# Kernel optimization log

Hardware: AMD Instinct MI355X
Metric: run time of the kernel (lower is better)

## Reference

```python
import jax, jax.numpy as jnp
import numpy as np
import math

B, S, D, H, MLP, L = 4, 1024, 512, 8, 2048, 4
C = D // H  # head dim = 64
K_RATIO = 0.25
TOPK = max(1, min(S, int(math.ceil(K_RATIO * S))))  # 256
EPS = 1e-6


def layernorm(x, w, b):
    mu = jnp.mean(x, axis=-1, keepdims=True)
    var = jnp.mean(jnp.square(x - mu), axis=-1, keepdims=True)
    return (x - mu) * jax.lax.rsqrt(var + EPS) * w + b


def dwconv3(x, w):
    # x: (B, Ch, S), w: (Ch, 1, 3) depthwise conv, padding 1
    return jax.lax.conv_general_dilated(
        x, w, window_strides=(1,), padding=[(1, 1)],
        dimension_numbers=('NCH', 'OIH', 'NCH'),
        feature_group_count=x.shape[1])


def setup_inputs() -> dict:
    key = jax.random.key(0)
    ks = jax.random.split(key, 16)
    g = lambda k, shape, s=0.02: jax.random.normal(k, shape, jnp.float32) * s
    return {
        'x': jax.random.normal(ks[0], (B, S, D), jnp.float32),
        'pos_emb': g(ks[1], (1, S, D)),
        'ln1_w': jnp.ones((L, D), jnp.float32),
        'ln1_b': jnp.zeros((L, D), jnp.float32),
        'qkv_w': g(ks[2], (L, 3 * D, D)),
        'dw_w': g(ks[3], (L, 3 * D, 1, 3), 0.1),
        'temp': jnp.ones((L, H), jnp.float32),
        'proj_w': g(ks[4], (L, D, D)),
        'ln2_w': jnp.ones((L, D), jnp.float32),
        'ln2_b': jnp.zeros((L, D), jnp.float32),
        'mlp_w1': g(ks[5], (L, MLP, D)),
        'mlp_b1': g(ks[6], (L, MLP), 1e-6),
        'mlp_w2': g(ks[7], (L, D, MLP)),
        'mlp_b2': g(ks[8], (L, D), 1e-6),
        'lnf_w': jnp.ones((D,), jnp.float32),
        'lnf_b': jnp.zeros((D,), jnp.float32),
    }


def _block(x, ln1_w, ln1_b, qkv_w, dw_w, temp, proj_w, ln2_w, ln2_b,
           mlp_w1, mlp_b1, mlp_w2, mlp_b2):
    # x: (B, S, D)
    h = layernorm(x, ln1_w, ln1_b).swapaxes(1, 2)        # (B, D, S)
    qkv = jnp.einsum('od,bds->bos', qkv_w, h)            # (B, 3D, S) 1x1 conv
    qkv = dwconv3(qkv, dw_w)                             # depthwise k=3
    q, k, v = jnp.split(qkv, 3, axis=1)                  # each (B, D, S)
    # 'b (head c) s -> b head s c'
    to_heads = lambda t: t.reshape(B, H, C, S).transpose(0, 1, 3, 2)
    q, k, v = to_heads(q), to_heads(k), to_heads(v)      # (B, H, S, C)
    q = q / jnp.maximum(jnp.linalg.norm(q, axis=-1, keepdims=True), 1e-12)
    k = k / jnp.maximum(jnp.linalg.norm(k, axis=-1, keepdims=True), 1e-12)
    scores = jnp.einsum('bhsc,bhtc->bhst', q, k) * temp[None, :, None, None]
    # top-k per query row: keep entries >= k-th largest, mask rest to -inf
    kth = jax.lax.top_k(scores, TOPK)[0][..., -1:]       # (B, H, S, 1)
    sparse = jnp.where(scores >= kth, scores, -jnp.inf)
    sparse = jnp.clip(sparse, -10000.0, 10000.0)         # -inf -> -10000
    attn = jax.nn.softmax(sparse, axis=-1)
    out = jnp.einsum('bhst,bhtc->bhsc', attn, v)         # (B, H, S, C)
    out = out.transpose(0, 1, 3, 2).reshape(B, D, S)     # 'b head s c -> b (head c) s'
    out = jnp.einsum('od,bds->bos', proj_w, out)         # project_out 1x1 conv
    x = x + out.swapaxes(1, 2)                           # residual (dropout=0)
    y = layernorm(x, ln2_w, ln2_b)
    y = jax.nn.gelu(y @ mlp_w1.T + mlp_b1, approximate=False) @ mlp_w2.T + mlp_b2
    return x + y


def reference(x, pos_emb, ln1_w, ln1_b, qkv_w, dw_w, temp, proj_w,
              ln2_w, ln2_b, mlp_w1, mlp_b1, mlp_w2, mlp_b2, lnf_w, lnf_b):
    h = x + pos_emb
    for i in range(L):
        h = _block(h, ln1_w[i], ln1_b[i], qkv_w[i], dw_w[i], temp[i], proj_w[i],
                   ln2_w[i], ln2_b[i], mlp_w1[i], mlp_b1[i], mlp_w2[i], mlp_b2[i])
    return layernorm(h, lnf_w, lnf_b)
```

## Files before the change

kernel.cpp:

```cpp
#include <hip/hip_runtime.h>

#define NB   4
#define SEQ  1024
#define DIM  512
#define NH   8
#define HD   64
#define MLPD 2048
#define NL   4
#define TOPKK 256
#define QKVD 1536
#define QT   16
#define SCB  1032

typedef short bh8 __attribute__((ext_vector_type(8)));
typedef float f32x4 __attribute__((ext_vector_type(4)));

__device__ __forceinline__ float b2f(unsigned short v) {
    return __uint_as_float(((unsigned)v) << 16);
}
__device__ __forceinline__ unsigned short f2b(float f) {
    unsigned u = __float_as_uint(f);
    u += 0x7FFFu + ((u >> 16) & 1u);
    return (unsigned short)(u >> 16);
}
__device__ __forceinline__ float ldin(const void* p, size_t i, int bf) {
    return bf ? b2f(((const unsigned short*)p)[i]) : ((const float*)p)[i];
}
__device__ __forceinline__ float wave_sum(float v) {
#pragma unroll
    for (int m = 32; m; m >>= 1) v += __shfl_xor(v, m);
    return v;
}
__device__ __forceinline__ unsigned f2key16(unsigned short u) {
    return (u & 0x8000u) ? (unsigned)((~u) & 0xFFFFu) : (unsigned)(u | 0x8000u);
}
__device__ __forceinline__ unsigned short key16b(unsigned k) {
    return (k & 0x8000u) ? (unsigned short)(k & 0x7FFFu)
                         : (unsigned short)((~k) & 0xFFFFu);
}
__device__ __forceinline__ uint4 pack8(const float* __restrict__ p) {
    uint4 r;
    r.x = (unsigned)f2b(p[0]) | ((unsigned)f2b(p[1]) << 16);
    r.y = (unsigned)f2b(p[2]) | ((unsigned)f2b(p[3]) << 16);
    r.z = (unsigned)f2b(p[4]) | ((unsigned)f2b(p[5]) << 16);
    r.w = (unsigned)f2b(p[6]) | ((unsigned)f2b(p[7]) << 16);
    return r;
}
__device__ __forceinline__ void async16(unsigned short* lds, const unsigned short* g) {
    __builtin_amdgcn_global_load_lds(
        (const __attribute__((address_space(1))) unsigned int*)g,
        (__attribute__((address_space(3))) unsigned int*)lds, 16, 0, 0);
}


__global__ void detect_kernel(const unsigned short* __restrict__ ln1w,
                              int* __restrict__ flag) {
    if (threadIdx.x == 0 && blockIdx.x == 0)
        *flag = (ln1w[0] == 0x3F80u) ? 1 : 0;
}

__global__ __launch_bounds__(256) void wcvt_kernel(
    const void* __restrict__ W, unsigned short* __restrict__ out,
    int n, const int* __restrict__ dflag) {
    int bf = *dflag;
    int idx = blockIdx.x * 256 + threadIdx.x;
    if (idx < n) out[idx] = f2b(ldin(W, idx, bf));
}

__global__ __launch_bounds__(256) void addpos_kernel(
    const void* __restrict__ x, const void* __restrict__ pos,
    float* __restrict__ h, const int* __restrict__ dflag) {
    int bf = *dflag;
    int idx = blockIdx.x * 256 + threadIdx.x;
    int sd = idx & (SEQ * DIM - 1);
    h[idx] = ldin(x, idx, bf) + ldin(pos, sd, bf);
}

__global__ __launch_bounds__(256) void ln_kernel(
    const float* __restrict__ in, const void* __restrict__ w,
    const void* __restrict__ bb, size_t wo, unsigned short* __restrict__ out,
    const int* __restrict__ dflag) {
    int bf = *dflag;
    __shared__ float red[4];
    int row = blockIdx.x, tid = threadIdx.x;
    int lane = tid & 63, wid = tid >> 6;
    const float* p = in + (size_t)row * DIM;
    float x0 = p[tid], x1 = p[tid + 256];
    float s = wave_sum(x0 + x1);
    if (!lane) red[wid] = s;
    __syncthreads();
    float mean = (red[0] + red[1] + red[2] + red[3]) * (1.0f / DIM);
    float d0 = x0 - mean, d1 = x1 - mean;
    float q = wave_sum(d0 * d0 + d1 * d1);
    __syncthreads();
    if (!lane) red[wid] = q;
    __syncthreads();
    float var = (red[0] + red[1] + red[2] + red[3]) * (1.0f / DIM);
    float rs = rsqrtf(var + 1e-6f);
    unsigned short* o = out + (size_t)row * DIM;
    o[tid]       = f2b(d0 * rs * ldin(w, wo + tid, bf) + ldin(bb, wo + tid, bf));
    o[tid + 256] = f2b(d1 * rs * ldin(w, wo + tid + 256, bf) + ldin(bb, wo + tid + 256, bf));
}

__global__ __launch_bounds__(256) void lnf_kernel(
    const float* __restrict__ in, const void* __restrict__ w,
    const void* __restrict__ bb, void* __restrict__ out,
    const int* __restrict__ dflag) {
    int bf = *dflag;
    __shared__ float red[4];
    int row = blockIdx.x, tid = threadIdx.x;
    int lane = tid & 63, wid = tid >> 6;
    const float* p = in + (size_t)row * DIM;
    float x0 = p[tid], x1 = p[tid + 256];
    float s = wave_sum(x0 + x1);
    if (!lane) red[wid] = s;
    __syncthreads();
    float mean = (red[0] + red[1] + red[2] + red[3]) * (1.0f / DIM);
    float d0 = x0 - mean, d1 = x1 - mean;
    float q = wave_sum(d0 * d0 + d1 * d1);
    __syncthreads();
    if (!lane) red[wid] = q;
    __syncthreads();
    float var = (red[0] + red[1] + red[2] + red[3]) * (1.0f / DIM);
    float rs = rsqrtf(var + 1e-6f);
    float v0 = d0 * rs * ldin(w, tid, bf) + ldin(bb, tid, bf);
    float v1 = d1 * rs * ldin(w, tid + 256, bf) + ldin(bb, tid + 256, bf);
    size_t o = (size_t)row * DIM;
    if (bf) {
        ((unsigned short*)out)[o + tid]       = f2b(v0);
        ((unsigned short*)out)[o + tid + 256] = f2b(v1);
    } else {
        ((float*)out)[o + tid]       = v0;
        ((float*)out)[o + tid + 256] = v1;
    }
}

__global__ __launch_bounds__(256) void gemm_mfma_kernel(
    const unsigned short* __restrict__ A, const void* __restrict__ W, size_t wo,
    const void* __restrict__ bias, size_t bo, void* __restrict__ C,
    int M, int N, int K, int flags, const int* __restrict__ dflag) {
    int bf = *dflag;
    __shared__ unsigned short As[128 * 32];
    __shared__ unsigned short Bs[128 * 32];
    int tid = threadIdx.x;
    int w = tid >> 6, l = tid & 63;
    int n0 = blockIdx.x * 128, m0 = blockIdx.y * 128;
    int wm = (w >> 1) * 64, wn = (w & 1) * 64;
    int lq = l & 15, lk = l >> 4;

    int srow = w * 32 + (l >> 2);
    int cb = (l & 3) * 8;
    const unsigned short* aG = A + (size_t)(m0 + srow) * K + cb;
    size_t wb = wo + (size_t)(n0 + srow) * K + cb;
    unsigned short* sA0 = &As[w * 1024 + l * 8];
    unsigned short* sA1 = &As[w * 1024 + 512 + l * 8];
    unsigned short* sB0 = &Bs[w * 1024 + l * 8];
    unsigned short* sB1 = &Bs[w * 1024 + 512 + l * 8];

    f32x4 acc[4][4];
#pragma unroll
    for (int i = 0; i < 4; ++i)
#pragma unroll
        for (int j = 0; j < 4; ++j)
            acc[i][j] = (f32x4){0.f, 0.f, 0.f, 0.f};

    for (int k0 = 0; k0 < K; k0 += 32) {
        uint4 a0 = *(const uint4*)(aG + k0);
        uint4 a1 = *(const uint4*)(aG + 16 * K + k0);
        uint4 b0, b1;
        if (bf) {
            b0 = *(const uint4*)((const unsigned short*)W + wb + k0);
            b1 = *(const uint4*)((const unsigned short*)W + wb + 16 * K + k0);
        } else {
            b0 = pack8((const float*)W + wb + k0);
            b1 = pack8((const float*)W + wb + 16 * K + k0);
        }
        __syncthreads();
        *(uint4*)sA0 = a0;
        *(uint4*)sA1 = a1;
        *(uint4*)sB0 = b0;
        *(uint4*)sB1 = b1;
        __syncthreads();
        bh8 af[4], bw[4];
#pragma unroll
        for (int i = 0; i < 4; ++i) {
            af[i] = *(const bh8*)&As[(wm + i * 16 + lq) * 32 + lk * 8];
            bw[i] = *(const bh8*)&Bs[(wn + i * 16 + lq) * 32 + lk * 8];
        }
#pragma unroll
        for (int i = 0; i < 4; ++i)
#pragma unroll
            for (int j = 0; j < 4; ++j)
                acc[i][j] = __builtin_amdgcn_mfma_f32_16x16x32_bf16(
                    af[i], bw[j], acc[i][j], 0, 0, 0);
    }

    int lr4 = lk * 4;
#pragma unroll
    for (int i = 0; i < 4; ++i) {
#pragma unroll
        for (int j = 0; j < 4; ++j) {
            int n = n0 + wn + j * 16 + lq;
            float bv = (flags & 4) ? ldin(bias, bo + n, bf) : 0.0f;
#pragma unroll
            for (int r = 0; r < 4; ++r) {
                int m = m0 + wm + i * 16 + lr4 + r;
                float v = acc[i][j][r] + bv;
                if (flags & 2) v = 0.5f * v * (1.0f + erff(v * 0.70710678118654752f));
                size_t o = (size_t)m * N + n;
                if (flags & 1) ((float*)C)[o] += v;
                else           ((unsigned short*)C)[o] = f2b(v);
            }
        }
    }
}

__global__ __launch_bounds__(256) void gemm_mfma_n64_kernel(
    const unsigned short* __restrict__ A, const void* __restrict__ W, size_t wo,
    const void* __restrict__ bias, size_t bo, void* __restrict__ C,
    int M, int N, int K, int flags, const int* __restrict__ dflag) {
    int bf = *dflag;
    __shared__ unsigned short As[128 * 32];
    __shared__ unsigned short Bs[64 * 32];
    int tid = threadIdx.x;
    int w = tid >> 6, l = tid & 63;
    int n0 = blockIdx.x * 64, m0 = blockIdx.y * 128;
    int wm = (w >> 1) * 64, wn = (w & 1) * 32;
    int lq = l & 15, lk = l >> 4;

    int srowA = w * 32 + (l >> 2);
    int cb = (l & 3) * 8;
    const unsigned short* aG = A + (size_t)(m0 + srowA) * K + cb;
    int srowB = w * 16 + (l >> 2);
    size_t wb = wo + (size_t)(n0 + srowB) * K + cb;
    unsigned short* sA0 = &As[w * 1024 + l * 8];
    unsigned short* sA1 = &As[w * 1024 + 512 + l * 8];
    unsigned short* sB0 = &Bs[w * 512 + l * 8];

    f32x4 acc[4][2];
#pragma unroll
    for (int i = 0; i < 4; ++i) {
        acc[i][0] = (f32x4){0.f, 0.f, 0.f, 0.f};
        acc[i][1] = (f32x4){0.f, 0.f, 0.f, 0.f};
    }

    for (int k0 = 0; k0 < K; k0 += 32) {
        uint4 a0 = *(const uint4*)(aG + k0);
        uint4 a1 = *(const uint4*)(aG + 16 * K + k0);
        uint4 b0;
        if (bf) b0 = *(const uint4*)((const unsigned short*)W + wb + k0);
        else    b0 = pack8((const float*)W + wb + k0);
        __syncthreads();
        *(uint4*)sA0 = a0;
        *(uint4*)sA1 = a1;
        *(uint4*)sB0 = b0;
        __syncthreads();
        bh8 af[4], bw[2];
#pragma unroll
        for (int i = 0; i < 4; ++i)
            af[i] = *(const bh8*)&As[(wm + i * 16 + lq) * 32 + lk * 8];
        bw[0] = *(const bh8*)&Bs[(wn + lq) * 32 + lk * 8];
        bw[1] = *(const bh8*)&Bs[(wn + 16 + lq) * 32 + lk * 8];
#pragma unroll
        for (int i = 0; i < 4; ++i) {
            acc[i][0] = __builtin_amdgcn_mfma_f32_16x16x32_bf16(af[i], bw[0], acc[i][0], 0, 0, 0);
            acc[i][1] = __builtin_amdgcn_mfma_f32_16x16x32_bf16(af[i], bw[1], acc[i][1], 0, 0, 0);
        }
    }

    int lr4 = lk * 4;
#pragma unroll
    for (int i = 0; i < 4; ++i) {
#pragma unroll
        for (int j = 0; j < 2; ++j) {
            int n = n0 + wn + j * 16 + lq;
            float bv = (flags & 4) ? ldin(bias, bo + n, bf) : 0.0f;
#pragma unroll
            for (int r = 0; r < 4; ++r) {
                int m = m0 + wm + i * 16 + lr4 + r;
                float v = acc[i][j][r] + bv;
                if (flags & 2) v = 0.5f * v * (1.0f + erff(v * 0.70710678118654752f));
                size_t o = (size_t)m * N + n;
                if (flags & 1) ((float*)C)[o] += v;
                else           ((unsigned short*)C)[o] = f2b(v);
            }
        }
    }
}

__global__ __launch_bounds__(256) void gemm_n64_dlds_kernel(
    const unsigned short* __restrict__ A, const unsigned short* __restrict__ W, size_t wo,
    const void* __restrict__ bias, size_t bo, void* __restrict__ C,
    int M, int N, int K, int flags, const int* __restrict__ dflag) {
    __shared__ unsigned short As[128 * 32];
    __shared__ unsigned short Bs[64 * 32];
    int tid = threadIdx.x;
    int w = tid >> 6, l = tid & 63;
    int n0 = blockIdx.x * 64, m0 = blockIdx.y * 128;
    int kz = blockIdx.z;
    int Ks = K / (int)gridDim.z;
    int kbeg = kz * Ks, kend = kbeg + Ks;
    int wm = (w >> 1) * 64, wn = (w & 1) * 32;
    int lq = l & 15, lk = l >> 4;

    int srowA = w * 32 + (l >> 2);
    int srowB = w * 16 + (l >> 2);
    int cb = (l & 3) * 8;
    const unsigned short* aG = A + (size_t)(m0 + srowA) * K + cb;
    const unsigned short* wG = W + wo + (size_t)(n0 + srowB) * K + cb;
    unsigned short* lA0 = As + w * 1024;
    unsigned short* lA1 = As + w * 1024 + 512;
    unsigned short* lB0 = Bs + w * 512;

    f32x4 acc[4][2];
#pragma unroll
    for (int i = 0; i < 4; ++i) {
        acc[i][0] = (f32x4){0.f, 0.f, 0.f, 0.f};
        acc[i][1] = (f32x4){0.f, 0.f, 0.f, 0.f};
    }

    for (int k0 = kbeg; k0 < kend; k0 += 32) {
        __syncthreads();
        async16(lA0, aG + k0);
        async16(lA1, aG + 16 * K + k0);
        async16(lB0, wG + k0);
        __syncthreads();
        bh8 af[4], bw[2];
#pragma unroll
        for (int i = 0; i < 4; ++i)
            af[i] = *(const bh8*)&As[(wm + i * 16 + lq) * 32 + lk * 8];
        bw[0] = *(const bh8*)&Bs[(wn + lq) * 32 + lk * 8];
        bw[1] = *(const bh8*)&Bs[(wn + 16 + lq) * 32 + lk * 8];
#pragma unroll
        for (int i = 0; i < 4; ++i) {
            acc[i][0] = __builtin_amdgcn_mfma_f32_16x16x32_bf16(af[i], bw[0], acc[i][0], 0, 0, 0);
            acc[i][1] = __builtin_amdgcn_mfma_f32_16x16x32_bf16(af[i], bw[1], acc[i][1], 0, 0, 0);
        }
    }

    int bf = (flags & 4) ? *dflag : 0;
    int lr4 = lk * 4;
#pragma unroll
    for (int i = 0; i < 4; ++i) {
#pragma unroll
        for (int j = 0; j < 2; ++j) {
            int n = n0 + wn + j * 16 + lq;
            float bv = ((flags & 4) && kz == 0) ? ldin(bias, bo + n, bf) : 0.0f;
#pragma unroll
            for (int r = 0; r < 4; ++r) {
                int m = m0 + wm + i * 16 + lr4 + r;
                float v = acc[i][j][r] + bv;
                if (flags & 2) v = 0.5f * v * (1.0f + erff(v * 0.70710678118654752f));
                size_t o = (size_t)m * N + n;
                if (flags & 8)      atomicAdd(&((float*)C)[o], v);
                else if (flags & 1) ((float*)C)[o] += v;
                else                ((unsigned short*)C)[o] = f2b(v);
            }
        }
    }
}

__global__ __launch_bounds__(256) void dwconv_kernel(
    const unsigned short* __restrict__ in, const void* __restrict__ w, size_t wo,
    unsigned short* __restrict__ out, const int* __restrict__ dflag) {
    int bf = *dflag;
    int idx = blockIdx.x * 256 + threadIdx.x;
    int o = idx % QKVD;
    int s = (idx / QKVD) & (SEQ - 1);
    float w0 = ldin(w, wo + o * 3 + 0, bf);
    float w1 = ldin(w, wo + o * 3 + 1, bf);
    float w2 = ldin(w, wo + o * 3 + 2, bf);
    float acc = w1 * b2f(in[idx]);
    if (s > 0)        acc += w0 * b2f(in[idx - QKVD]);
    if (s < SEQ - 1)  acc += w2 * b2f(in[idx + QKVD]);
    out[idx] = f2b(acc);
}

__global__ __launch_bounds__(256) void qkvprep_kernel(
    unsigned short* __restrict__ qkv, const void* __restrict__ temp, size_t to,
    unsigned short* __restrict__ Kc, unsigned short* __restrict__ Vt,
    const int* __restrict__ dflag) {
    int bf = *dflag;
    int tid = threadIdx.x;
    int g = tid >> 6, c = tid & 63;
    int gid = blockIdx.x * 4 + g;
    int h = gid & 7;
    int bs = gid >> 3;
    int s = bs & (SEQ - 1), b = bs >> 10;
    int bh = b * NH + h;
    unsigned short* p = qkv + (size_t)bs * QKVD + h * HD;
    float qv = b2f(p[c]), kv = b2f(p[512 + c]);
    float qs = wave_sum(qv * qv);
    float ks = wave_sum(kv * kv);
    float t = ldin(temp, to + h, bf);
    p[c] = f2b(qv / fmaxf(sqrtf(qs), 1e-12f) * t);
    Kc[((size_t)bh * SEQ + s) * HD + c] = f2b(kv / fmaxf(sqrtf(ks), 1e-12f));
    Vt[(((size_t)bh * 32 + (s >> 5)) * HD + c) * 32 + (s & 31)] = p[1024 + c];
}

__global__ __launch_bounds__(256) void attn_kernel(
    const unsigned short* __restrict__ qkv, const unsigned short* __restrict__ Kc,
    const unsigned short* __restrict__ Vt, unsigned short* __restrict__ outp) {
    __shared__ unsigned short sc16[QT * SCB];
    __shared__ float inv16[QT];

    int tid = threadIdx.x;
    int w = tid >> 6, l = tid & 63;
    int lq = l & 15, lk = l >> 4;
    int bid = blockIdx.x;
    int qt = bid & 63;
    int h = (bid >> 6) & 7;
    int b = bid >> 9;
    int bh = b * NH + h;

    const unsigned short* base = qkv + (size_t)b * SEQ * QKVD;

    const unsigned short* qp = base + (size_t)(qt * QT + lq) * QKVD + h * HD + lk * 8;
    bh8 aq0 = *(const bh8*)(qp);
    bh8 aq1 = *(const bh8*)(qp + 32);

    const unsigned short* Kbh = Kc + (size_t)bh * SEQ * HD;
    for (int kb = 0; kb < 16; ++kb) {
        int key0 = (w * 16 + kb) * 16;
        const unsigned short* kp = Kbh + (size_t)(key0 + lq) * HD + lk * 8;
        bh8 b0 = *(const bh8*)(kp);
        bh8 b1 = *(const bh8*)(kp + 32);
        f32x4 acc = {0.f, 0.f, 0.f, 0.f};
        acc = __builtin_amdgcn_mfma_f32_16x16x32_bf16(aq0, b0, acc, 0, 0, 0);
        acc = __builtin_amdgcn_mfma_f32_16x16x32_bf16(aq1, b1, acc, 0, 0, 0);
        sc16[(lk * 4 + 0) * SCB + key0 + lq] = f2b(acc[0]);
        sc16[(lk * 4 + 1) * SCB + key0 + lq] = f2b(acc[1]);
        sc16[(lk * 4 + 2) * SCB + key0 + lq] = f2b(acc[2]);
        sc16[(lk * 4 + 3) * SCB + key0 + lq] = f2b(acc[3]);
    }
    __syncthreads();

    for (int rr = 0; rr < 4; ++rr) {
        int row = w * 4 + rr;
        unsigned short* srow = sc16 + row * SCB;
        uint4 r0 = *(const uint4*)&srow[l * 8];
        uint4 r1 = *(const uint4*)&srow[512 + l * 8];
        unsigned wd[8] = {r0.x, r0.y, r0.z, r0.w, r1.x, r1.y, r1.z, r1.w};
        float v[16];
#pragma unroll
        for (int j = 0; j < 8; ++j) {
            v[2 * j]     = __uint_as_float(wd[j] << 16);
            v[2 * j + 1] = __uint_as_float(wd[j] & 0xFFFF0000u);
        }
        float m = v[0];
#pragma unroll
        for (int j = 1; j < 16; ++j) m = fmaxf(m, v[j]);
#pragma unroll
        for (int off = 1; off < 64; off <<= 1) m = fmaxf(m, __shfl_xor(m, off));
        m = fminf(fmaxf(m, -10000.f), 10000.f);
        unsigned T = 0;
        for (int bit = 15; bit >= 0; --bit) {
            unsigned cand = T | (1u << bit);
            float tf = b2f(key16b(cand));
            unsigned cnt = 0;
#pragma unroll
            for (int j = 0; j < 16; ++j)
                cnt += (unsigned)__popcll(__ballot(v[j] >= tf));
            if (cnt >= TOPKK) T = cand;
        }
        float kth = b2f(key16b(T));
        float e[16];
        float ssum = 0.f;
#pragma unroll
        for (int j = 0; j < 16; ++j) {
            float a = fminf(fmaxf(v[j], -10000.f), 10000.f);
            float ev = (v[j] >= kth) ? __expf(a - m) : 0.0f;
            ssum += ev;
            e[j] = ev;
        }
#pragma unroll
        for (int off = 1; off < 64; off <<= 1) ssum += __shfl_xor(ssum, off);
        if (l == 0) inv16[row] = 1.0f / ssum;
        unsigned pw[8];
#pragma unroll
        for (int j = 0; j < 8; ++j) {
            unsigned r;
            asm("v_cvt_pk_bf16_f32 %0, %1, %2" : "=v"(r) : "v"(e[2 * j]), "v"(e[2 * j + 1]));
            pw[j] = r;
        }
        *(uint4*)&srow[l * 8]       = (uint4){pw[0], pw[1], pw[2], pw[3]};
        *(uint4*)&srow[512 + l * 8] = (uint4){pw[4], pw[5], pw[6], pw[7]};
    }
    __syncthreads();

    {
        const unsigned short* Vbh = Vt + (size_t)bh * SEQ * HD;
        const unsigned short* prow = sc16 + lq * SCB;
        f32x4 oacc = {0.f, 0.f, 0.f, 0.f};
        for (int tc = 0; tc < 32; ++tc) {
            bh8 ap = *(const bh8*)&prow[tc * 32 + lk * 8];
            bh8 bv = *(const bh8*)(Vbh + (size_t)tc * 2048 + (w * 16 + lq) * 32 + lk * 8);
            oacc = __builtin_amdgcn_mfma_f32_16x16x32_bf16(ap, bv, oacc, 0, 0, 0);
        }
#pragma unroll
        for (int r = 0; r < 4; ++r) {
            int q = lk * 4 + r;
            float val = oacc[r] * inv16[q];
            outp[((size_t)(b * SEQ + qt * QT + q)) * DIM + h * HD + w * 16 + lq] = f2b(val);
        }
    }
}

extern "C" void kernel_launch(void* const* d_in, const int* in_sizes, int n_in,
                              void* d_out, int out_size, void* d_ws, size_t ws_size,
                              hipStream_t stream) {
    (void)in_sizes; (void)n_in; (void)out_size;
    const void* x     = d_in[0];
    const void* pos   = d_in[1];
    const void* ln1w  = d_in[2];
    const void* ln1b  = d_in[3];
    const void* qkvw  = d_in[4];
    const void* dww   = d_in[5];
    const void* temp  = d_in[6];
    const void* projw = d_in[7];
    const void* ln2w  = d_in[8];
    const void* ln2b  = d_in[9];
    const void* w1    = d_in[10];
    const void* b1    = d_in[11];
    const void* w2    = d_in[12];
    const void* b2    = d_in[13];
    const void* lnfw  = d_in[14];
    const void* lnfb  = d_in[15];

    float* wsf = (float*)d_ws;
    const size_t M1 = (size_t)1024 * 1024;
    float*          h    = wsf;
    unsigned short* bn   = (unsigned short*)(wsf + 2 * M1);
    unsigned short* C2   = (unsigned short*)(wsf + 3 * M1);
    unsigned short* C1   = (unsigned short*)(wsf + 6 * M1);
    unsigned short* Vt   = (unsigned short*)(wsf + 6 * M1);
    unsigned short* Kc   = (unsigned short*)(wsf + 7 * M1);
    unsigned short* Mb   = C2;
    int*            flag = (int*)(wsf + 9 * M1);
    unsigned short* Wc   = (unsigned short*)(wsf + 9 * M1 + 16);

    const int MTOK  = NB * SEQ;
    const int nQKVW = NL * QKVD * DIM;
    const int nPROJ = NL * DIM * DIM;
    const int nW1   = NL * MLPD * DIM;
    const int nW2   = NL * DIM * MLPD;
    const size_t wcElems = (size_t)nQKVW + nPROJ + nW1 + nW2;
    const int big = ws_size >= ((9 * M1 + 16) * 4 + wcElems * 2);

    unsigned short* WcQ  = Wc;
    unsigned short* WcP  = Wc + nQKVW;
    unsigned short* WcW1 = Wc + nQKVW + nPROJ;
    unsigned short* WcW2 = Wc + nQKVW + nPROJ + (size_t)nW1;

    detect_kernel<<<1, 64, 0, stream>>>((const unsigned short*)ln1w, flag);
    addpos_kernel<<<(NB * SEQ * DIM) / 256, 256, 0, stream>>>(x, pos, h, flag);

    if (big) {
        wcvt_kernel<<<nQKVW / 256, 256, 0, stream>>>(qkvw, WcQ, nQKVW, flag);
        wcvt_kernel<<<nPROJ / 256, 256, 0, stream>>>(projw, WcP, nPROJ, flag);
        wcvt_kernel<<<nW1 / 256, 256, 0, stream>>>(w1, WcW1, nW1, flag);
        wcvt_kernel<<<nW2 / 256, 256, 0, stream>>>(w2, WcW2, nW2, flag);
    }

    for (int l = 0; l < NL; ++l) {
        ln_kernel<<<MTOK, 256, 0, stream>>>(h, ln1w, ln1b, (size_t)l * DIM, bn, flag);
        if (big) {
            gemm_n64_dlds_kernel<<<dim3(QKVD / 64, MTOK / 128, 1), 256, 0, stream>>>(
                bn, WcQ, (size_t)l * QKVD * DIM, nullptr, 0, C1,
                MTOK, QKVD, DIM, 0, flag);
        } else {
            gemm_mfma_kernel<<<dim3(QKVD / 128, MTOK / 128), 256, 0, stream>>>(
                bn, qkvw, (size_t)l * QKVD * DIM, nullptr, 0, C1,
                MTOK, QKVD, DIM, 0, flag);
        }
        dwconv_kernel<<<(NB * SEQ * QKVD) / 256, 256, 0, stream>>>(
            C1, dww, (size_t)l * QKVD * 3, C2, flag);
        qkvprep_kernel<<<(NB * SEQ * NH) / 4, 256, 0, stream>>>(
            C2, temp, (size_t)l * NH, Kc, Vt, flag);
        attn_kernel<<<NB * NH * (SEQ / QT), 256, 0, stream>>>(C2, Kc, Vt, bn);
        if (big) {
            gemm_n64_dlds_kernel<<<dim3(DIM / 64, MTOK / 128, 2), 256, 0, stream>>>(
                bn, WcP, (size_t)l * DIM * DIM, nullptr, 0, h,
                MTOK, DIM, DIM, 8, flag);
        } else {
            gemm_mfma_n64_kernel<<<dim3(DIM / 64, MTOK / 128), 256, 0, stream>>>(
                bn, projw, (size_t)l * DIM * DIM, nullptr, 0, h,
                MTOK, DIM, DIM, 1, flag);
        }
        ln_kernel<<<MTOK, 256, 0, stream>>>(h, ln2w, ln2b, (size_t)l * DIM, bn, flag);
        if (big) {
            gemm_n64_dlds_kernel<<<dim3(MLPD / 64, MTOK / 128, 1), 256, 0, stream>>>(
                bn, WcW1, (size_t)l * MLPD * DIM, b1, (size_t)l * MLPD, Mb,
                MTOK, MLPD, DIM, 2 | 4, flag);
            gemm_n64_dlds_kernel<<<dim3(DIM / 64, MTOK / 128, 2), 256, 0, stream>>>(
                Mb, WcW2, (size_t)l * DIM * MLPD, b2, (size_t)l * DIM, h,
                MTOK, DIM, MLPD, 8 | 4, flag);
        } else {
            gemm_mfma_kernel<<<dim3(MLPD / 128, MTOK / 128), 256, 0, stream>>>(
                bn, w1, (size_t)l * MLPD * DIM, b1, (size_t)l * MLPD, Mb,
                MTOK, MLPD, DIM, 2 | 4, flag);
            gemm_mfma_n64_kernel<<<dim3(DIM / 64, MTOK / 128), 256, 0, stream>>>(
                Mb, w2, (size_t)l * DIM * MLPD, b2, (size_t)l * DIM, h,
                MTOK, DIM, MLPD, 1 | 4, flag);
        }
    }

    lnf_kernel<<<MTOK, 256, 0, stream>>>(h, lnfw, lnfb, d_out, flag);
}
```

Measured before the change: 1.045 ms.

## Fuse depthwise conv into QKV prep and swizzle attention score LDS layout

Merges the depthwise k=3 conv and the q/k normalisation/V transpose into a single kernel. Normalised q is now written to a compact buffer that the attention kernel reads, which removes one full bf16 round trip of the QKV tensor per layer and one launch. In the attention kernel the padded score rows are replaced by an XOR-swizzled unpadded LDS layout to avoid bank conflicts. Softmax normalisation is applied to the probabilities before the bf16 pack instead of after PV, which slightly changes rounding. The attention kernel reads q from the same buffer it writes its output to; this relies on each block reading its q tile before it writes.

```diff
diff --git a/kernel.cpp b/kernel.cpp
--- a/kernel.cpp
+++ b/kernel.cpp
@@ -10,7 +10,6 @@
 #define TOPKK 256
 #define QKVD 1536
 #define QT   16
-#define SCB  1032
 
 typedef short bh8 __attribute__((ext_vector_type(8)));
 typedef float f32x4 __attribute__((ext_vector_type(4)));
@@ -360,26 +359,11 @@
     }
 }
 
-__global__ __launch_bounds__(256) void dwconv_kernel(
+__global__ __launch_bounds__(256) void dwqkv_kernel(
     const unsigned short* __restrict__ in, const void* __restrict__ w, size_t wo,
-    unsigned short* __restrict__ out, const int* __restrict__ dflag) {
-    int bf = *dflag;
-    int idx = blockIdx.x * 256 + threadIdx.x;
-    int o = idx % QKVD;
-    int s = (idx / QKVD) & (SEQ - 1);
-    float w0 = ldin(w, wo + o * 3 + 0, bf);
-    float w1 = ldin(w, wo + o * 3 + 1, bf);
-    float w2 = ldin(w, wo + o * 3 + 2, bf);
-    float acc = w1 * b2f(in[idx]);
-    if (s > 0)        acc += w0 * b2f(in[idx - QKVD]);
-    if (s < SEQ - 1)  acc += w2 * b2f(in[idx + QKVD]);
-    out[idx] = f2b(acc);
-}
-
-__global__ __launch_bounds__(256) void qkvprep_kernel(
-    unsigned short* __restrict__ qkv, const void* __restrict__ temp, size_t to,
-    unsigned short* __restrict__ Kc, unsigned short* __restrict__ Vt,
-    const int* __restrict__ dflag) {
+    const void* __restrict__ temp, size_t to,
+    unsigned short* __restrict__ qn, unsigned short* __restrict__ Kc,
+    unsigned short* __restrict__ Vt, const int* __restrict__ dflag) {
     int bf = *dflag;
     int tid = threadIdx.x;
     int g = tid >> 6, c = tid & 63;
@@ -388,21 +372,31 @@
     int bs = gid >> 3;
     int s = bs & (SEQ - 1), b = bs >> 10;
     int bh = b * NH + h;
-    unsigned short* p = qkv + (size_t)bs * QKVD + h * HD;
-    float qv = b2f(p[c]), kv = b2f(p[512 + c]);
-    float qs = wave_sum(qv * qv);
-    float ks = wave_sum(kv * kv);
-    float t = ldin(temp, to + h, bf);
-    p[c] = f2b(qv / fmaxf(sqrtf(qs), 1e-12f) * t);
-    Kc[((size_t)bh * SEQ + s) * HD + c] = f2b(kv / fmaxf(sqrtf(ks), 1e-12f));
-    Vt[(((size_t)bh * 32 + (s >> 5)) * HD + c) * 32 + (s & 31)] = p[1024 + c];
+    const unsigned short* row = in + (size_t)bs * QKVD;
+    float vals[3];
+#pragma unroll
+    for (int t = 0; t < 3; ++t) {
+        int o = t * 512 + h * HD + c;
+        float w0 = ldin(w, wo + o * 3 + 0, bf);
+        float w1 = ldin(w, wo + o * 3 + 1, bf);
+        float w2 = ldin(w, wo + o * 3 + 2, bf);
+        float a = w1 * b2f(row[o]);
+        if (s > 0)       a += w0 * b2f(row[o - QKVD]);
+        if (s < SEQ - 1) a += w2 * b2f(row[o + QKVD]);
+        vals[t] = a;
+    }
+    float qs = wave_sum(vals[0] * vals[0]);
+    float ks = wave_sum(vals[1] * vals[1]);
+    float t_ = ldin(temp, to + h, bf);
+    qn[(size_t)bs * DIM + h * HD + c] = f2b(vals[0] / fmaxf(sqrtf(qs), 1e-12f) * t_);
+    Kc[((size_t)bh * SEQ + s) * HD + c] = f2b(vals[1] / fmaxf(sqrtf(ks), 1e-12f));
+    Vt[(((size_t)bh * 32 + (s >> 5)) * HD + c) * 32 + (s & 31)] = f2b(vals[2]);
 }
 
 __global__ __launch_bounds__(256) void attn_kernel(
-    const unsigned short* __restrict__ qkv, const unsigned short* __restrict__ Kc,
+    const unsigned short* __restrict__ q, const unsigned short* __restrict__ Kc,
     const unsigned short* __restrict__ Vt, unsigned short* __restrict__ outp) {
-    __shared__ unsigned short sc16[QT * SCB];
-    __shared__ float inv16[QT];
+    __shared__ __align__(16) unsigned short sc16[QT * 1024];
 
     int tid = threadIdx.x;
     int w = tid >> 6, l = tid & 63;
@@ -413,13 +407,12 @@
     int b = bid >> 9;
     int bh = b * NH + h;
 
-    const unsigned short* base = qkv + (size_t)b * SEQ * QKVD;
-
-    const unsigned short* qp = base + (size_t)(qt * QT + lq) * QKVD + h * HD + lk * 8;
+    const unsigned short* qp = q + (size_t)(b * SEQ + qt * QT + lq) * DIM + h * HD + lk * 8;
     bh8 aq0 = *(const bh8*)(qp);
     bh8 aq1 = *(const bh8*)(qp + 32);
 
     const unsigned short* Kbh = Kc + (size_t)bh * SEQ * HD;
+    int wi = lq & 7;
     for (int kb = 0; kb < 16; ++kb) {
         int key0 = (w * 16 + kb) * 16;
         const unsigned short* kp = Kbh + (size_t)(key0 + lq) * HD + lk * 8;
@@ -428,16 +421,19 @@
         f32x4 acc = {0.f, 0.f, 0.f, 0.f};
         acc = __builtin_amdgcn_mfma_f32_16x16x32_bf16(aq0, b0, acc, 0, 0, 0);
         acc = __builtin_amdgcn_mfma_f32_16x16x32_bf16(aq1, b1, acc, 0, 0, 0);
-        sc16[(lk * 4 + 0) * SCB + key0 + lq] = f2b(acc[0]);
-        sc16[(lk * 4 + 1) * SCB + key0 + lq] = f2b(acc[1]);
-        sc16[(lk * 4 + 2) * SCB + key0 + lq] = f2b(acc[2]);
-        sc16[(lk * 4 + 3) * SCB + key0 + lq] = f2b(acc[3]);
+        int chunk = (key0 + lq) >> 3;
+#pragma unroll
+        for (int r = 0; r < 4; ++r) {
+            int row = lk * 4 + r;
+            int sw = (row ^ (row >> 2)) & 7;
+            sc16[row * 1024 + ((chunk ^ sw) << 3) + wi] = f2b(acc[r]);
+        }
     }
     __syncthreads();
 
     for (int rr = 0; rr < 4; ++rr) {
         int row = w * 4 + rr;
-        unsigned short* srow = sc16 + row * SCB;
+        unsigned short* srow = sc16 + row * 1024;
         uint4 r0 = *(const uint4*)&srow[l * 8];
         uint4 r1 = *(const uint4*)&srow[512 + l * 8];
         unsigned wd[8] = {r0.x, r0.y, r0.z, r0.w, r1.x, r1.y, r1.z, r1.w};
@@ -464,23 +460,23 @@
             if (cnt >= TOPKK) T = cand;
         }
         float kth = b2f(key16b(T));
-        float e[16];
         float ssum = 0.f;
 #pragma unroll
         for (int j = 0; j < 16; ++j) {
             float a = fminf(fmaxf(v[j], -10000.f), 10000.f);
             float ev = (v[j] >= kth) ? __expf(a - m) : 0.0f;
             ssum += ev;
-            e[j] = ev;
+            v[j] = ev;
         }
 #pragma unroll
         for (int off = 1; off < 64; off <<= 1) ssum += __shfl_xor(ssum, off);
-        if (l == 0) inv16[row] = 1.0f / ssum;
+        float inv = 1.0f / ssum;
         unsigned pw[8];
 #pragma unroll
         for (int j = 0; j < 8; ++j) {
+            float e0 = v[2 * j] * inv, e1 = v[2 * j + 1] * inv;
             unsigned r;
-            asm("v_cvt_pk_bf16_f32 %0, %1, %2" : "=v"(r) : "v"(e[2 * j]), "v"(e[2 * j + 1]));
+            asm("v_cvt_pk_bf16_f32 %0, %1, %2" : "=v"(r) : "v"(e0), "v"(e1));
             pw[j] = r;
         }
         *(uint4*)&srow[l * 8]       = (uint4){pw[0], pw[1], pw[2], pw[3]};
@@ -490,18 +486,18 @@
 
     {
         const unsigned short* Vbh = Vt + (size_t)bh * SEQ * HD;
-        const unsigned short* prow = sc16 + lq * SCB;
+        const unsigned short* prow = sc16 + lq * 1024;
+        int swq = (lq ^ (lq >> 2)) & 7;
         f32x4 oacc = {0.f, 0.f, 0.f, 0.f};
         for (int tc = 0; tc < 32; ++tc) {
-            bh8 ap = *(const bh8*)&prow[tc * 32 + lk * 8];
+            bh8 ap = *(const bh8*)&prow[((tc * 4 + lk) ^ swq) << 3];
             bh8 bv = *(const bh8*)(Vbh + (size_t)tc * 2048 + (w * 16 + lq) * 32 + lk * 8);
             oacc = __builtin_amdgcn_mfma_f32_16x16x32_bf16(ap, bv, oacc, 0, 0, 0);
         }
 #pragma unroll
         for (int r = 0; r < 4; ++r) {
-            int q = lk * 4 + r;
-            float val = oacc[r] * inv16[q];
-            outp[((size_t)(b * SEQ + qt * QT + q)) * DIM + h * HD + w * 16 + lq] = f2b(val);
+            int qrow = lk * 4 + r;
+            outp[((size_t)(b * SEQ + qt * QT + qrow)) * DIM + h * HD + w * 16 + lq] = f2b(oacc[r]);
         }
     }
 }
@@ -532,7 +528,6 @@
     float*          h    = wsf;
     unsigned short* bn   = (unsigned short*)(wsf + 2 * M1);
     unsigned short* C2   = (unsigned short*)(wsf + 3 * M1);
-    unsigned short* C1   = (unsigned short*)(wsf + 6 * M1);
     unsigned short* Vt   = (unsigned short*)(wsf + 6 * M1);
     unsigned short* Kc   = (unsigned short*)(wsf + 7 * M1);
     unsigned short* Mb   = C2;
@@ -566,18 +561,16 @@
         ln_kernel<<<MTOK, 256, 0, stream>>>(h, ln1w, ln1b, (size_t)l * DIM, bn, flag);
         if (big) {
             gemm_n64_dlds_kernel<<<dim3(QKVD / 64, MTOK / 128, 1), 256, 0, stream>>>(
-                bn, WcQ, (size_t)l * QKVD * DIM, nullptr, 0, C1,
+                bn, WcQ, (size_t)l * QKVD * DIM, nullptr, 0, C2,
                 MTOK, QKVD, DIM, 0, flag);
         } else {
             gemm_mfma_kernel<<<dim3(QKVD / 128, MTOK / 128), 256, 0, stream>>>(
-                bn, qkvw, (size_t)l * QKVD * DIM, nullptr, 0, C1,
+                bn, qkvw, (size_t)l * QKVD * DIM, nullptr, 0, C2,
                 MTOK, QKVD, DIM, 0, flag);
         }
-        dwconv_kernel<<<(NB * SEQ * QKVD) / 256, 256, 0, stream>>>(
-            C1, dww, (size_t)l * QKVD * 3, C2, flag);
-        qkvprep_kernel<<<(NB * SEQ * NH) / 4, 256, 0, stream>>>(
-            C2, temp, (size_t)l * NH, Kc, Vt, flag);
-        attn_kernel<<<NB * NH * (SEQ / QT), 256, 0, stream>>>(C2, Kc, Vt, bn);
+        dwqkv_kernel<<<(NB * SEQ * NH) / 4, 256, 0, stream>>>(
+            C2, dww, (size_t)l * QKVD * 3, temp, (size_t)l * NH, bn, Kc, Vt, flag);
+        attn_kernel<<<NB * NH * (SEQ / QT), 256, 0, stream>>>(bn, Kc, Vt, bn);
         if (big) {
             gemm_n64_dlds_kernel<<<dim3(DIM / 64, MTOK / 128, 2), 256, 0, stream>>>(
                 bn, WcP, (size_t)l * DIM * DIM, nullptr, 0, h,
```

Measured after the change: 1.014 ms. 1.03x faster.
